# Performance work log

Measured on AMD Instinct MI355X. Metric: run time of the kernel, lower is better.

Reference implementation:

```python
import jax, jax.numpy as jnp
import numpy as np
import math

D_MODEL = 512
N_HEADS = 8
D_K = D_MODEL // N_HEADS
B, S, KC = 16, 1024, 32
NEG = -1e32


def setup_inputs() -> dict:
    key = jax.random.key(0)
    ks = jax.random.split(key, 14)
    s = 1.0 / math.sqrt(D_MODEL)
    return {
        "q": jax.random.normal(ks[0], (B, S, D_MODEL), jnp.float32),
        "k": jax.random.normal(ks[1], (B, S, D_MODEL), jnp.float32),
        "v": jax.random.normal(ks[2], (B, S, D_MODEL), jnp.float32),
        "q_seq": jax.random.randint(ks[3], (B, S), 0, 500, jnp.int32),
        "c_seq": jax.random.randint(ks[4], (B, S, KC), 0, 2, jnp.int32),
        "Wq": jax.random.normal(ks[5], (D_MODEL, D_MODEL), jnp.float32) * s,
        "bq": jnp.zeros((D_MODEL,), jnp.float32),
        "Wk": jax.random.normal(ks[6], (D_MODEL, D_MODEL), jnp.float32) * s,
        "bk": jnp.zeros((D_MODEL,), jnp.float32),
        "Wv": jax.random.normal(ks[7], (D_MODEL, D_MODEL), jnp.float32) * s,
        "bv": jnp.zeros((D_MODEL,), jnp.float32),
        "Wo": jax.random.normal(ks[8], (D_MODEL, D_MODEL), jnp.float32) * s,
        "bo": jnp.zeros((D_MODEL,), jnp.float32),
    }


def qc_mask(q_seq, c_seq):
    # maskq[b,i,j] = 1 if same question id
    maskq = (q_seq[:, :, None] == q_seq[:, None, :]).astype(jnp.int32)
    # maskc[b,i,j] = 1 if any shared concept; entries are {0,1} so AND-sum == dot
    overlap = jnp.einsum("bik,bjk->bij", c_seq, c_seq)  # int32
    maskc = (overlap > 0).astype(jnp.int32)
    # strict lower triangle: 1 - triu(ones, k=0)
    tri = jnp.tril(jnp.ones((S, S), jnp.int32), k=-1)[None]
    return (maskc + maskq + 1) * tri  # values in {0,1,2,3}


def reference(q, k, v, q_seq, c_seq, Wq, bq, Wk, bk, Wv, bv, Wo, bo):
    bs = q.shape[0]
    # NOTE: original code swaps the linears: k<-k_linear(k), q<-v_linear(q), v<-q_linear(v)
    kh = (k @ Wk.T + bk).reshape(bs, S, N_HEADS, D_K).transpose(0, 2, 1, 3)
    qh = (q @ Wv.T + bv).reshape(bs, S, N_HEADS, D_K).transpose(0, 2, 1, 3)
    vh = (v @ Wq.T + bq).reshape(bs, S, N_HEADS, D_K).transpose(0, 2, 1, 3)

    mask = qc_mask(q_seq, c_seq)  # [B,S,S] int
    scores = jnp.einsum("bhid,bhjd->bhij", qh, kh) / math.sqrt(D_K)
    m = mask[:, None]  # [B,1,S,S]
    scores = jnp.where(m == 0, NEG, scores)
    scores = jax.nn.softmax(scores, axis=-1)

    adjustments = jnp.array([0.0, 0.5, 1.0, 2.0], jnp.float32)
    adjusted = scores * adjustments[m]
    sums = jnp.sum(scores, axis=-1, keepdims=True)
    sums = jnp.where(sums == 0, jnp.ones_like(sums), sums)
    adjusted = adjusted / sums

    out = jnp.einsum("bhij,bhjd->bhid", adjusted, vh)
    concat = out.transpose(0, 2, 1, 3).reshape(bs, S, D_MODEL)
    return concat @ Wo.T + bo
```

## Files before the change

kernel.cpp:

```cpp
#include <hip/hip_runtime.h>
#include <stdint.h>

typedef unsigned short u16;
typedef unsigned int   u32;
typedef unsigned long long u64;
typedef __attribute__((ext_vector_type(8)))  short short8;
typedef __attribute__((ext_vector_type(4)))  float f32x4;
typedef __attribute__((ext_vector_type(16))) float f32x16;
typedef __attribute__((ext_vector_type(4)))  unsigned int u32x4;

__device__ __forceinline__ u16 f2bf(float f) {
  u32 u = __builtin_bit_cast(u32, f);
  u32 r = u + 0x7FFFu + ((u >> 16) & 1u);
  return (u16)(r >> 16);
}

__device__ __forceinline__ u32 cvtpk(float a, float b) {
  u32 r;
  asm("v_cvt_pk_bf16_f32 %0, %1, %2" : "=v"(r) : "v"(a), "v"(b));
  return r;
}

__device__ __forceinline__ void gload_lds16(const void* g, void* l) {
  __builtin_amdgcn_global_load_lds(
      (__attribute__((address_space(1))) void*)(uintptr_t)g,
      (__attribute__((address_space(3))) void*)(u32)(uintptr_t)l,
      16, 0, 0);
}

__global__ void cast4_kernel(const float* __restrict__ s0, const float* __restrict__ s1,
                             const float* __restrict__ s2, const float* __restrict__ s3,
                             u16* __restrict__ d0, u16* __restrict__ d1,
                             u16* __restrict__ d2, u16* __restrict__ d3, int n8) {
  const int sel = blockIdx.y;
  const float* src = sel == 0 ? s0 : sel == 1 ? s1 : sel == 2 ? s2 : s3;
  u16* dst = sel == 0 ? d0 : sel == 1 ? d1 : sel == 2 ? d2 : d3;
  int i = blockIdx.x * blockDim.x + threadIdx.x;
  if (i >= n8) return;
  const float4* s4 = (const float4*)src;
  float4 x = s4[2 * (size_t)i];
  float4 y = s4[2 * (size_t)i + 1];
  u32x4 r;
  r.x = cvtpk(x.x, x.y); r.y = cvtpk(x.z, x.w);
  r.z = cvtpk(y.x, y.y); r.w = cvtpk(y.z, y.w);
  *(u32x4*)(dst + 8 * (size_t)i) = r;
}

__global__ void pack_kernel(const int* __restrict__ q_seq, const int* __restrict__ c_seq,
                            int2* __restrict__ meta, int n) {
  int i = blockIdx.x * blockDim.x + threadIdx.x;
  if (i >= n) return;
  u32 bits = 0;
#pragma unroll
  for (int j = 0; j < 32; ++j)
    bits |= (c_seq[(size_t)i * 32 + j] != 0) ? (1u << j) : 0u;
  meta[i] = make_int2(q_seq[i], (int)bits);
}

__global__ __launch_bounds__(256) void mask_kernel(const int2* __restrict__ meta,
                                                   u64* __restrict__ maskw) {
  const int qc = blockIdx.x, kt = blockIdx.y, b = blockIdx.z;
  const int t = threadIdx.x;
  const int q = qc * 256 + t;
  __shared__ int2 colm[32];
  if (t < 32) colm[t] = meta[b * 1024 + kt * 32 + t];
  __syncthreads();
  const int2 qm = meta[b * 1024 + q];
  const int rs = qm.x; const u32 rb = (u32)qm.y;
  u64 w = 0;
#pragma unroll
  for (int j = 0; j < 32; ++j) {
    const int2 cm = colm[j];
    const int kj = kt * 32 + j;
    u32 m = 0;
    if (kj < q) m = 1u + (rs == cm.x ? 1u : 0u) + (((rb & (u32)cm.y) != 0u) ? 1u : 0u);
    w |= (u64)m << (2 * j);
  }
  maskw[((size_t)b * 32 + kt) * 1024 + q] = w;
}

__global__ __launch_bounds__(256) void gemm_qkv(const float* __restrict__ qf,
                                                const float* __restrict__ kf,
                                                const float* __restrict__ vf,
                                                const u16* __restrict__ Wvb,
                                                const u16* __restrict__ Wkb,
                                                const u16* __restrict__ Wqb,
                                                const float* __restrict__ bv,
                                                const float* __restrict__ bk,
                                                const float* __restrict__ bq,
                                                u16* __restrict__ qhb,
                                                u16* __restrict__ khb,
                                                u16* __restrict__ vTb,
                                                float kscale) {
  const int sel = blockIdx.y;
  const float* Af   = sel == 0 ? qf : sel == 1 ? kf : vf;
  const u16*   W    = sel == 0 ? Wvb : sel == 1 ? Wkb : Wqb;
  const float* bias = sel == 0 ? bv : sel == 1 ? bk : bq;
  const float scale = sel == 1 ? kscale : 1.0f;
  const int K = 512;

  __shared__ __align__(16) u16 As[128 * 64];
  __shared__ __align__(16) u16 Bs[128 * 64];
  const int t    = threadIdx.x;
  const int lane = t & 63;
  const int wid  = t >> 6;
  const int g    = lane >> 4, l15 = lane & 15;
  const int wm   = wid >> 1, wn = wid & 1;
  const int wrk  = (blockIdx.x & 7) * 64 + (blockIdx.x >> 3);
  const int mb   = wrk >> 2, nbi = wrk & 3;
  const int m0   = mb << 7, n0 = nbi << 7;
  const int srow = t >> 3;
  const int scol = (((t & 7) ^ (srow & 7)) << 3);
  const int rsw  = l15 & 7;

  f32x4 acc[4][4];
#pragma unroll
  for (int i = 0; i < 4; ++i)
#pragma unroll
    for (int j = 0; j < 4; ++j) acc[i][j] = f32x4{0.f, 0.f, 0.f, 0.f};

  float4 ax[4], ay[4];
#pragma unroll
  for (int i = 0; i < 4; ++i) {
    const float* src = Af + (size_t)(m0 + 32 * i + srow) * K + scol;
    ax[i] = *(const float4*)src;
    ay[i] = *(const float4*)(src + 4);
  }

  for (int k0 = 0; k0 < K; k0 += 64) {
    __builtin_amdgcn_sched_barrier(0);
    __builtin_amdgcn_s_barrier();
    __builtin_amdgcn_sched_barrier(0);
#pragma unroll
    for (int i = 0; i < 4; ++i)
      gload_lds16(W + (size_t)(n0 + i * 32 + srow) * K + k0 + scol,
                  Bs + i * 2048 + t * 8);
#pragma unroll
    for (int i = 0; i < 4; ++i) {
      u32x4 r;
      r.x = cvtpk(ax[i].x, ax[i].y); r.y = cvtpk(ax[i].z, ax[i].w);
      r.z = cvtpk(ay[i].x, ay[i].y); r.w = cvtpk(ay[i].z, ay[i].w);
      *(u32x4*)(As + (32 * i + srow) * 64 + ((t & 7) << 3)) = r;
    }
    __builtin_amdgcn_sched_barrier(0);
    const int kn = (k0 + 64) & (K - 1);
#pragma unroll
    for (int i = 0; i < 4; ++i) {
      const float* src = Af + (size_t)(m0 + 32 * i + srow) * K + kn + scol;
      ax[i] = *(const float4*)src;
      ay[i] = *(const float4*)(src + 4);
    }
    __builtin_amdgcn_sched_barrier(0);
    asm volatile("s_waitcnt vmcnt(8) lgkmcnt(0)" ::: "memory");
    __builtin_amdgcn_s_barrier();
    __builtin_amdgcn_sched_barrier(0);
#pragma unroll
    for (int kk = 0; kk < 2; ++kk) {
      short8 a[4], b[4];
#pragma unroll
      for (int mi = 0; mi < 4; ++mi)
        a[mi] = *(const short8*)(As + (wm * 64 + mi * 16 + l15) * 64
                                 + (((kk * 4 + g) ^ rsw) << 3));
#pragma unroll
      for (int ni = 0; ni < 4; ++ni)
        b[ni] = *(const short8*)(Bs + (wn * 64 + ni * 16 + l15) * 64
                                 + (((kk * 4 + g) ^ rsw) << 3));
#pragma unroll
      for (int mi = 0; mi < 4; ++mi)
#pragma unroll
        for (int ni = 0; ni < 4; ++ni)
          acc[mi][ni] = __builtin_amdgcn_mfma_f32_16x16x32_bf16(a[mi], b[ni], acc[mi][ni], 0, 0, 0);
    }
  }
  asm volatile("s_waitcnt vmcnt(0)" ::: "memory");

#pragma unroll
  for (int ni = 0; ni < 4; ++ni) {
    const int col = n0 + wn * 64 + ni * 16 + l15;
    const float bz = bias[col];
#pragma unroll
    for (int mi = 0; mi < 4; ++mi) {
#pragma unroll
      for (int r = 0; r < 4; ++r) {
        const int row = m0 + wm * 64 + mi * 16 + g * 4 + r;
        const u16 val = f2bf((acc[mi][ni][r] + bz) * scale);
        const size_t base = ((size_t)(row >> 10) * 8 + (col >> 6)) * 65536;
        const int s = row & 1023, d = col & 63;
        if (sel == 0) {
          qhb[base + (size_t)s * 64 + d] = val;
        } else if (sel == 1) {
          khb[base + (s >> 5) * 2048 + (d >> 3) * 256 + (s & 31) * 8 + (d & 7)] = val;
        } else {
          vTb[base + (s >> 3) * 512 + d * 8 + (s & 7)] = val;
        }
      }
    }
  }
}

__global__ __launch_bounds__(256) void gemm_out(const u16* __restrict__ A,
                                                const u16* __restrict__ W,
                                                const float* __restrict__ bias,
                                                float* __restrict__ outp) {
  const int K = 512, N = 512;
  __shared__ __align__(16) u16 As[128 * 64];
  __shared__ __align__(16) u16 Bs[128 * 64];
  const int t    = threadIdx.x;
  const int lane = t & 63;
  const int wid  = t >> 6;
  const int g    = lane >> 4, l15 = lane & 15;
  const int wm   = wid >> 1, wn = wid & 1;
  const int wrk  = (blockIdx.x & 7) * 64 + (blockIdx.x >> 3);
  const int mb   = wrk >> 2, nbi = wrk & 3;
  const int m0   = mb << 7, n0 = nbi << 7;
  const int srow = t >> 3;
  const int scol = (((t & 7) ^ (srow & 7)) << 3);
  const int rsw  = l15 & 7;

  f32x4 acc[4][4];
#pragma unroll
  for (int i = 0; i < 4; ++i)
#pragma unroll
    for (int j = 0; j < 4; ++j) acc[i][j] = f32x4{0.f, 0.f, 0.f, 0.f};

  for (int k0 = 0; k0 < K; k0 += 64) {
    __builtin_amdgcn_sched_barrier(0);
    __builtin_amdgcn_s_barrier();
    __builtin_amdgcn_sched_barrier(0);
#pragma unroll
    for (int i = 0; i < 4; ++i) {
      gload_lds16(A + (size_t)(m0 + i * 32 + srow) * K + k0 + scol, As + i * 2048 + t * 8);
      gload_lds16(W + (size_t)(n0 + i * 32 + srow) * K + k0 + scol, Bs + i * 2048 + t * 8);
    }
    __builtin_amdgcn_sched_barrier(0);
    asm volatile("s_waitcnt vmcnt(0)" ::: "memory");
    __builtin_amdgcn_s_barrier();
    __builtin_amdgcn_sched_barrier(0);
#pragma unroll
    for (int kk = 0; kk < 2; ++kk) {
      short8 a[4], b[4];
#pragma unroll
      for (int mi = 0; mi < 4; ++mi)
        a[mi] = *(const short8*)(As + (wm * 64 + mi * 16 + l15) * 64
                                 + (((kk * 4 + g) ^ rsw) << 3));
#pragma unroll
      for (int ni = 0; ni < 4; ++ni)
        b[ni] = *(const short8*)(Bs + (wn * 64 + ni * 16 + l15) * 64
                                 + (((kk * 4 + g) ^ rsw) << 3));
#pragma unroll
      for (int mi = 0; mi < 4; ++mi)
#pragma unroll
        for (int ni = 0; ni < 4; ++ni)
          acc[mi][ni] = __builtin_amdgcn_mfma_f32_16x16x32_bf16(a[mi], b[ni], acc[mi][ni], 0, 0, 0);
    }
  }

#pragma unroll
  for (int ni = 0; ni < 4; ++ni) {
    const int col = n0 + wn * 64 + ni * 16 + l15;
    const float bz = bias[col];
#pragma unroll
    for (int mi = 0; mi < 4; ++mi)
#pragma unroll
      for (int r = 0; r < 4; ++r) {
        const int row = m0 + wm * 64 + mi * 16 + g * 4 + r;
        outp[(size_t)row * N + col] = acc[mi][ni][r] + bz;
      }
  }
}

__global__ __launch_bounds__(256, 4) void attn_kernel(const u16* __restrict__ qh,
                                                      const u16* __restrict__ kh,
                                                      const u16* __restrict__ vT,
                                                      const u64* __restrict__ maskw,
                                                      u16* __restrict__ outc) {
  const int h  = blockIdx.x;
  const int qp = blockIdx.y;
  const int b  = blockIdx.z;
  const int lane = threadIdx.x & 63;
  const int wid  = threadIdx.x >> 6;
  const int pair = wid >> 1, p = wid & 1;
  const int l31 = lane & 31;
  const int hh  = lane >> 5;
  const int hh8 = hh << 3, fourh = hh << 2, eighth = hh << 3;
  const int jt = pair ? (31 - qp) : qp;
  const int q0 = jt << 5;
  const int qi = q0 + l31;
  const size_t bh = (size_t)b * 8 + h;
  const u16* Q  = qh + bh * 65536;
  const u16* Kp = kh + bh * 65536;
  const u16* Vt = vT + bh * 65536;
  const u64* mrow = maskw + (size_t)b * 32768 + qi;

  __shared__ float mO[2][32][64];
  __shared__ float mL[2][64];
  __shared__ __align__(16) float Sl[2][32];

  short8 qB[4];
#pragma unroll
  for (int i = 0; i < 4; ++i)
    qB[i] = *(const short8*)(Q + (size_t)qi * 64 + i * 16 + eighth);

  f32x16 O0, O1;
#pragma unroll
  for (int i = 0; i < 16; ++i) { O0[i] = 0.f; O1[i] = 0.f; }
  float lr[4] = {0.f, 0.f, 0.f, 0.f};

  const int nt = jt + 1;

  short8 kA[4];
#pragma unroll
  for (int i = 0; i < 4; ++i)
    kA[i] = *(const short8*)(Kp + p * 2048 + ((2 * i + hh) * 32 + l31) * 8);
  u64 wm = mrow[(size_t)p << 10];

  for (int t = p; t < nt; t += 2) {
    const int k0 = t << 5;

    f32x16 S;
#pragma unroll
    for (int i = 0; i < 16; ++i) S[i] = 0.f;
#pragma unroll
    for (int i = 0; i < 4; ++i)
      S = __builtin_amdgcn_mfma_f32_32x32x16_bf16(kA[i], qB[i], S, 0, 0, 0);

    u64 wmn = 0;
    if (t + 2 < nt) {
#pragma unroll
      for (int i = 0; i < 4; ++i)
        kA[i] = *(const short8*)(Kp + (t + 2) * 2048 + ((2 * i + hh) * 32 + l31) * 8);
      wmn = mrow[(size_t)(t + 2) << 10];
    }

    short8 vB[2][2];
#pragma unroll
    for (int t4 = 0; t4 < 2; ++t4)
#pragma unroll
      for (int j = 0; j < 2; ++j)
        vB[t4][j] = *(const short8*)(Vt + (size_t)(t * 4 + t4 * 2 + hh) * 512 + (32 * j + l31) * 8);

    const u32 wsh0 = ((u32)wm) >> hh8;
    const u32 wsh1 = ((u32)(wm >> 32)) >> hh8;
    u32 pk[8];
#pragma unroll
    for (int s = 0; s < 4; ++s) {
      const u32 wsel = (s < 2) ? wsh0 : wsh1;
      float pv[4];
#pragma unroll
      for (int r = 0; r < 4; ++r) {
        const int m = 4 * s + r;
        const u32 m2 = (wsel >> (2 * r + 16 * (s & 1))) & 3u;
        float e;
        asm("v_exp_f32 %0, %1" : "=v"(e) : "v"(S[m]));
        const float pp = (m2 != 0u) ? e : 0.f;
        lr[r] += pp;
        asm("v_ldexp_f32 %0, %1, %2" : "=v"(pv[r]) : "v"(pp), "v"(m2));
      }
      pk[2 * s]     = cvtpk(pv[0], pv[1]);
      pk[2 * s + 1] = cvtpk(pv[2], pv[3]);
    }
    wm = wmn;

#pragma unroll
    for (int t4 = 0; t4 < 2; ++t4) {
      u32 a0 = pk[4 * t4 + 0], b0 = pk[4 * t4 + 2];
      u32 a1 = pk[4 * t4 + 1], b1 = pk[4 * t4 + 3];
      asm("v_permlane32_swap_b32 %0, %1" : "+v"(a0), "+v"(b0));
      asm("v_permlane32_swap_b32 %0, %1" : "+v"(a1), "+v"(b1));
      u32x4 w; w.x = a0; w.y = a1; w.z = b0; w.w = b1;
      const short8 pa = __builtin_bit_cast(short8, w);
      O0 = __builtin_amdgcn_mfma_f32_32x32x16_bf16(pa, vB[t4][0], O0, 0, 0, 0);
      O1 = __builtin_amdgcn_mfma_f32_32x32x16_bf16(pa, vB[t4][1], O1, 0, 0, 0);
    }
  }

  float lrun = (lr[0] + lr[1]) + (lr[2] + lr[3]);

  if (p == 1) {
#pragma unroll
    for (int r = 0; r < 16; ++r) {
      mO[pair][r][lane]      = O0[r];
      mO[pair][16 + r][lane] = O1[r];
    }
    mL[pair][lane] = lrun;
  }
  __syncthreads();
  if (p == 0) {
#pragma unroll
    for (int r = 0; r < 16; ++r) {
      O0[r] += mO[pair][r][lane];
      O1[r] += mO[pair][16 + r][lane];
    }
    lrun += mL[pair][lane];

    const float ssum = lrun + __shfl_xor(lrun, 32);
    if (lane < 32) Sl[pair][l31] = (ssum > 0.f) ? 0.25f / ssum : 0.f;
    __builtin_amdgcn_sched_barrier(0);
    asm volatile("s_waitcnt lgkmcnt(0)" ::: "memory");
    __builtin_amdgcn_sched_barrier(0);
#pragma unroll
    for (int t2 = 0; t2 < 4; ++t2) {
      const float4 inv4 = *(const float4*)&Sl[pair][8 * t2 + fourh];
#pragma unroll
      for (int r = 0; r < 4; ++r) {
        const int m = 4 * t2 + r;
        const float iv = (r == 0) ? inv4.x : (r == 1) ? inv4.y : (r == 2) ? inv4.z : inv4.w;
        const int qrow = q0 + 8 * t2 + fourh + r;
        u16* op = outc + ((size_t)b * 1024 + qrow) * 512 + h * 64;
        op[l31]      = f2bf(O0[m] * iv);
        op[32 + l31] = f2bf(O1[m] * iv);
      }
    }
  }
}

extern "C" void kernel_launch(void* const* d_in, const int* in_sizes, int n_in,
                              void* d_out, int out_size, void* d_ws, size_t ws_size,
                              hipStream_t stream) {
  (void)in_sizes; (void)n_in; (void)out_size; (void)ws_size;
  const float* q    = (const float*)d_in[0];
  const float* k    = (const float*)d_in[1];
  const float* v    = (const float*)d_in[2];
  const int*  q_seq = (const int*)d_in[3];
  const int*  c_seq = (const int*)d_in[4];
  const float* Wq   = (const float*)d_in[5];
  const float* bq   = (const float*)d_in[6];
  const float* Wk   = (const float*)d_in[7];
  const float* bk   = (const float*)d_in[8];
  const float* Wv   = (const float*)d_in[9];
  const float* bv   = (const float*)d_in[10];
  const float* Wo   = (const float*)d_in[11];
  const float* bo   = (const float*)d_in[12];
  float* out = (float*)d_out;

  char* ws = (char*)d_ws;
  const size_t SZH = 16ull * 8 * 1024 * 64 * 2;
  u16* qhb   = (u16*)(ws + 0 * SZH);
  u16* khb   = (u16*)(ws + 1 * SZH);
  u16* vTb   = (u16*)(ws + 2 * SZH);
  u16* attnc = (u16*)(ws + 3 * SZH);
  u16* Wvb = (u16*)(ws + 4 * SZH + 0 * 524288);
  u16* Wkb = (u16*)(ws + 4 * SZH + 1 * 524288);
  u16* Wqb = (u16*)(ws + 4 * SZH + 2 * 524288);
  u16* Wob = (u16*)(ws + 4 * SZH + 3 * 524288);
  int2* meta  = (int2*)(ws + 4 * SZH + 4 * 524288);
  u64* maskw  = (u64*)(ws + 4 * SZH + 4 * 524288 + 131072);

  const int n8w = 512 * 512 / 8;
  cast4_kernel<<<dim3(n8w / 256, 4), 256, 0, stream>>>(Wv, Wk, Wq, Wo,
                                                       Wvb, Wkb, Wqb, Wob, n8w);
  pack_kernel<<<64, 256, 0, stream>>>(q_seq, c_seq, meta, 16384);
  mask_kernel<<<dim3(4, 32, 16), 256, 0, stream>>>(meta, maskw);

  const float KSCALE = 0.18033688011112042f;
  gemm_qkv<<<dim3(512, 3), 256, 0, stream>>>(q, k, v, Wvb, Wkb, Wqb,
                                             bv, bk, bq, qhb, khb, vTb, KSCALE);
  attn_kernel<<<dim3(8, 16, 16), 256, 0, stream>>>(qhb, khb, vTb, maskw, attnc);
  gemm_out<<<512, 256, 0, stream>>>(attnc, Wob, bo, out);
}
```

Before: 142.6 us.

## Double-buffer LDS tiles in QKV and output projection GEMMs

Both projection GEMMs now keep two LDS buffers for the A and B tiles. The next k-tile's global-to-LDS loads are issued before the MFMAs on the current tile, so each iteration needs one barrier instead of two. This is meant to hide global load latency behind matrix math. In exchange, LDS use per block doubles to 64 KB, which may lower occupancy.

After: 145.1 us. Within noise of the previous version (+1.8%).

```diff
diff --git a/kernel.cpp b/kernel.cpp
--- a/kernel.cpp
+++ b/kernel.cpp
@@ -27,6 +27,8 @@
       (__attribute__((address_space(3))) void*)(u32)(uintptr_t)l,
       16, 0, 0);
 }
+
+#define SB() __builtin_amdgcn_sched_barrier(0)
 
 __global__ void cast4_kernel(const float* __restrict__ s0, const float* __restrict__ s1,
                              const float* __restrict__ s2, const float* __restrict__ s3,
@@ -99,8 +101,8 @@
   const float scale = sel == 1 ? kscale : 1.0f;
   const int K = 512;
 
-  __shared__ __align__(16) u16 As[128 * 64];
-  __shared__ __align__(16) u16 Bs[128 * 64];
+  __shared__ __align__(16) u16 As[2][128 * 64];
+  __shared__ __align__(16) u16 Bs[2][128 * 64];
   const int t    = threadIdx.x;
   const int lane = t & 63;
   const int wid  = t >> 6;
@@ -111,6 +113,7 @@
   const int m0   = mb << 7, n0 = nbi << 7;
   const int srow = t >> 3;
   const int scol = (((t & 7) ^ (srow & 7)) << 3);
+  const int dcol = ((t & 7) << 3);
   const int rsw  = l15 & 7;
 
   f32x4 acc[4][4];
@@ -126,51 +129,97 @@
     ax[i] = *(const float4*)src;
     ay[i] = *(const float4*)(src + 4);
   }
-
-  for (int k0 = 0; k0 < K; k0 += 64) {
-    __builtin_amdgcn_sched_barrier(0);
-    __builtin_amdgcn_s_barrier();
-    __builtin_amdgcn_sched_barrier(0);
+  SB();
+#pragma unroll
+  for (int i = 0; i < 4; ++i)
+    gload_lds16(W + (size_t)(n0 + i * 32 + srow) * K + scol, &Bs[0][i * 2048 + t * 8]);
+  SB();
+  asm volatile("s_waitcnt vmcnt(4)" ::: "memory");
+#pragma unroll
+  for (int i = 0; i < 4; ++i) {
+    u32x4 r;
+    r.x = cvtpk(ax[i].x, ax[i].y); r.y = cvtpk(ax[i].z, ax[i].w);
+    r.z = cvtpk(ay[i].x, ay[i].y); r.w = cvtpk(ay[i].z, ay[i].w);
+    *(u32x4*)(&As[0][(32 * i + srow) * 64 + dcol]) = r;
+  }
+  SB();
+#pragma unroll
+  for (int i = 0; i < 4; ++i) {
+    const float* src = Af + (size_t)(m0 + 32 * i + srow) * K + 64 + scol;
+    ax[i] = *(const float4*)src;
+    ay[i] = *(const float4*)(src + 4);
+  }
+  SB();
+  asm volatile("s_waitcnt vmcnt(8) lgkmcnt(0)" ::: "memory");
+  __builtin_amdgcn_s_barrier();
+  SB();
+
+  for (int tt = 0; tt < 7; ++tt) {
+    const int c = tt & 1;
+    const u16* Asc = As[c];
+    const u16* Bsc = Bs[c];
+    u16* Asn = As[c ^ 1];
+    u16* Bsn = Bs[c ^ 1];
 #pragma unroll
     for (int i = 0; i < 4; ++i)
-      gload_lds16(W + (size_t)(n0 + i * 32 + srow) * K + k0 + scol,
-                  Bs + i * 2048 + t * 8);
+      gload_lds16(W + (size_t)(n0 + i * 32 + srow) * K + (tt + 1) * 64 + scol,
+                  Bsn + i * 2048 + t * 8);
+    SB();
 #pragma unroll
     for (int i = 0; i < 4; ++i) {
       u32x4 r;
       r.x = cvtpk(ax[i].x, ax[i].y); r.y = cvtpk(ax[i].z, ax[i].w);
       r.z = cvtpk(ay[i].x, ay[i].y); r.w = cvtpk(ay[i].z, ay[i].w);
-      *(u32x4*)(As + (32 * i + srow) * 64 + ((t & 7) << 3)) = r;
-    }
-    __builtin_amdgcn_sched_barrier(0);
-    const int kn = (k0 + 64) & (K - 1);
+      *(u32x4*)(Asn + (32 * i + srow) * 64 + dcol) = r;
+    }
+    SB();
+    const int kn = ((tt + 2) & 7) * 64;
 #pragma unroll
     for (int i = 0; i < 4; ++i) {
       const float* src = Af + (size_t)(m0 + 32 * i + srow) * K + kn + scol;
       ax[i] = *(const float4*)src;
       ay[i] = *(const float4*)(src + 4);
     }
-    __builtin_amdgcn_sched_barrier(0);
+    SB();
+#pragma unroll
+    for (int kk = 0; kk < 2; ++kk) {
+      short8 a[4], b[4];
+#pragma unroll
+      for (int mi = 0; mi < 4; ++mi)
+        a[mi] = *(const short8*)(Asc + (wm * 64 + mi * 16 + l15) * 64
+                                 + (((kk * 4 + g) ^ rsw) << 3));
+#pragma unroll
+      for (int ni = 0; ni < 4; ++ni)
+        b[ni] = *(const short8*)(Bsc + (wn * 64 + ni * 16 + l15) * 64
+                                 + (((kk * 4 + g) ^ rsw) << 3));
+#pragma unroll
+      for (int mi = 0; mi < 4; ++mi)
+#pragma unroll
+        for (int ni = 0; ni < 4; ++ni)
+          acc[mi][ni] = __builtin_amdgcn_mfma_f32_16x16x32_bf16(a[mi], b[ni], acc[mi][ni], 0, 0, 0);
+    }
+    SB();
     asm volatile("s_waitcnt vmcnt(8) lgkmcnt(0)" ::: "memory");
     __builtin_amdgcn_s_barrier();
-    __builtin_amdgcn_sched_barrier(0);
-#pragma unroll
-    for (int kk = 0; kk < 2; ++kk) {
-      short8 a[4], b[4];
-#pragma unroll
-      for (int mi = 0; mi < 4; ++mi)
-        a[mi] = *(const short8*)(As + (wm * 64 + mi * 16 + l15) * 64
-                                 + (((kk * 4 + g) ^ rsw) << 3));
+    SB();
+  }
+
+#pragma unroll
+  for (int kk = 0; kk < 2; ++kk) {
+    short8 a[4], b[4];
+#pragma unroll
+    for (int mi = 0; mi < 4; ++mi)
+      a[mi] = *(const short8*)(&As[1][(wm * 64 + mi * 16 + l15) * 64
+                               + (((kk * 4 + g) ^ rsw) << 3)]);
+#pragma unroll
+    for (int ni = 0; ni < 4; ++ni)
+      b[ni] = *(const short8*)(&Bs[1][(wn * 64 + ni * 16 + l15) * 64
+                               + (((kk * 4 + g) ^ rsw) << 3)]);
+#pragma unroll
+    for (int mi = 0; mi < 4; ++mi)
 #pragma unroll
       for (int ni = 0; ni < 4; ++ni)
-        b[ni] = *(const short8*)(Bs + (wn * 64 + ni * 16 + l15) * 64
-                                 + (((kk * 4 + g) ^ rsw) << 3));
-#pragma unroll
-      for (int mi = 0; mi < 4; ++mi)
-#pragma unroll
-        for (int ni = 0; ni < 4; ++ni)
-          acc[mi][ni] = __builtin_amdgcn_mfma_f32_16x16x32_bf16(a[mi], b[ni], acc[mi][ni], 0, 0, 0);
-    }
+        acc[mi][ni] = __builtin_amdgcn_mfma_f32_16x16x32_bf16(a[mi], b[ni], acc[mi][ni], 0, 0, 0);
   }
   asm volatile("s_waitcnt vmcnt(0)" ::: "memory");
 
@@ -203,8 +252,8 @@
                                                 const float* __restrict__ bias,
                                                 float* __restrict__ outp) {
   const int K = 512, N = 512;
-  __shared__ __align__(16) u16 As[128 * 64];
-  __shared__ __align__(16) u16 Bs[128 * 64];
+  __shared__ __align__(16) u16 As[2][128 * 64];
+  __shared__ __align__(16) u16 Bs[2][128 * 64];
   const int t    = threadIdx.x;
   const int lane = t & 63;
   const int wid  = t >> 6;
@@ -223,29 +272,40 @@
 #pragma unroll
     for (int j = 0; j < 4; ++j) acc[i][j] = f32x4{0.f, 0.f, 0.f, 0.f};
 
-  for (int k0 = 0; k0 < K; k0 += 64) {
-    __builtin_amdgcn_sched_barrier(0);
-    __builtin_amdgcn_s_barrier();
-    __builtin_amdgcn_sched_barrier(0);
+#pragma unroll
+  for (int i = 0; i < 4; ++i) {
+    gload_lds16(A + (size_t)(m0 + i * 32 + srow) * K + scol, &As[0][i * 2048 + t * 8]);
+    gload_lds16(W + (size_t)(n0 + i * 32 + srow) * K + scol, &Bs[0][i * 2048 + t * 8]);
+  }
+  SB();
+  asm volatile("s_waitcnt vmcnt(0)" ::: "memory");
+  __builtin_amdgcn_s_barrier();
+  SB();
+
+  for (int tt = 0; tt < 7; ++tt) {
+    const int c = tt & 1;
+    const u16* Asc = As[c];
+    const u16* Bsc = Bs[c];
+    u16* Asn = As[c ^ 1];
+    u16* Bsn = Bs[c ^ 1];
 #pragma unroll
     for (int i = 0; i < 4; ++i) {
-      gload_lds16(A + (size_t)(m0 + i * 32 + srow) * K + k0 + scol, As + i * 2048 + t * 8);
-      gload_lds16(W + (size_t)(n0 + i * 32 + srow) * K + k0 + scol, Bs + i * 2048 + t * 8);
-    }
-    __builtin_amdgcn_sched_barrier(0);
-    asm volatile("s_waitcnt vmcnt(0)" ::: "memory");
-    __builtin_amdgcn_s_barrier();
-    __builtin_amdgcn_sched_barrier(0);
+      gload_lds16(A + (size_t)(m0 + i * 32 + srow) * K + (tt + 1) * 64 + scol,
+                  Asn + i * 2048 + t * 8);
+      gload_lds16(W + (size_t)(n0 + i * 32 + srow) * K + (tt + 1) * 64 + scol,
+                  Bsn + i * 2048 + t * 8);
+    }
+    SB();
 #pragma unroll
     for (int kk = 0; kk < 2; ++kk) {
       short8 a[4], b[4];
 #pragma unroll
       for (int mi = 0; mi < 4; ++mi)
-        a[mi] = *(const short8*)(As + (wm * 64 + mi * 16 + l15) * 64
+        a[mi] = *(const short8*)(Asc + (wm * 64 + mi * 16 + l15) * 64
                                  + (((kk * 4 + g) ^ rsw) << 3));
 #pragma unroll
       for (int ni = 0; ni < 4; ++ni)
-        b[ni] = *(const short8*)(Bs + (wn * 64 + ni * 16 + l15) * 64
+        b[ni] = *(const short8*)(Bsc + (wn * 64 + ni * 16 + l15) * 64
                                  + (((kk * 4 + g) ^ rsw) << 3));
 #pragma unroll
       for (int mi = 0; mi < 4; ++mi)
@@ -253,6 +313,28 @@
         for (int ni = 0; ni < 4; ++ni)
           acc[mi][ni] = __builtin_amdgcn_mfma_f32_16x16x32_bf16(a[mi], b[ni], acc[mi][ni], 0, 0, 0);
     }
+    SB();
+    asm volatile("s_waitcnt vmcnt(0) lgkmcnt(0)" ::: "memory");
+    __builtin_amdgcn_s_barrier();
+    SB();
+  }
+
+#pragma unroll
+  for (int kk = 0; kk < 2; ++kk) {
+    short8 a[4], b[4];
+#pragma unroll
+    for (int mi = 0; mi < 4; ++mi)
+      a[mi] = *(const short8*)(&As[1][(wm * 64 + mi * 16 + l15) * 64
+                               + (((kk * 4 + g) ^ rsw) << 3)]);
+#pragma unroll
+    for (int ni = 0; ni < 4; ++ni)
+      b[ni] = *(const short8*)(&Bs[1][(wn * 64 + ni * 16 + l15) * 64
+                               + (((kk * 4 + g) ^ rsw) << 3)]);
+#pragma unroll
+    for (int mi = 0; mi < 4; ++mi)
+#pragma unroll
+      for (int ni = 0; ni < 4; ++ni)
+        acc[mi][ni] = __builtin_amdgcn_mfma_f32_16x16x32_bf16(a[mi], b[ni], acc[mi][ni], 0, 0, 0);
   }
 
 #pragma unroll
```

## Process two key tiles per attention loop iteration with double-buffered K loads

Applied to the files above, without the earlier changes.

The attention inner loop now handles two key tiles (t and t+2) per iteration, with separate K-fragment and mask buffers, and prefetches the next pair before the softmax and PV work. V fragments are now loaded inside the PV step instead of up front. The aim is more independent MFMA and exp work in flight to hide load and dependency latency. To fit the extra registers, launch bounds drop from 4 to 2 blocks per CU, which risks lower occupancy. Adding the SB() macro and hoisting the store column into dcol are cosmetic.

Result: no change. 140.1 us (-1.7%).

```diff
diff --git a/kernel.cpp b/kernel.cpp
--- a/kernel.cpp
+++ b/kernel.cpp
@@ -27,6 +27,8 @@
       (__attribute__((address_space(3))) void*)(u32)(uintptr_t)l,
       16, 0, 0);
 }
+
+#define SB() __builtin_amdgcn_sched_barrier(0)
 
 __global__ void cast4_kernel(const float* __restrict__ s0, const float* __restrict__ s1,
                              const float* __restrict__ s2, const float* __restrict__ s3,
@@ -111,6 +113,7 @@
   const int m0   = mb << 7, n0 = nbi << 7;
   const int srow = t >> 3;
   const int scol = (((t & 7) ^ (srow & 7)) << 3);
+  const int dcol = ((t & 7) << 3);
   const int rsw  = l15 & 7;
 
   f32x4 acc[4][4];
@@ -128,9 +131,9 @@
   }
 
   for (int k0 = 0; k0 < K; k0 += 64) {
-    __builtin_amdgcn_sched_barrier(0);
+    SB();
     __builtin_amdgcn_s_barrier();
-    __builtin_amdgcn_sched_barrier(0);
+    SB();
 #pragma unroll
     for (int i = 0; i < 4; ++i)
       gload_lds16(W + (size_t)(n0 + i * 32 + srow) * K + k0 + scol,
@@ -140,9 +143,9 @@
       u32x4 r;
       r.x = cvtpk(ax[i].x, ax[i].y); r.y = cvtpk(ax[i].z, ax[i].w);
       r.z = cvtpk(ay[i].x, ay[i].y); r.w = cvtpk(ay[i].z, ay[i].w);
-      *(u32x4*)(As + (32 * i + srow) * 64 + ((t & 7) << 3)) = r;
-    }
-    __builtin_amdgcn_sched_barrier(0);
+      *(u32x4*)(As + (32 * i + srow) * 64 + dcol) = r;
+    }
+    SB();
     const int kn = (k0 + 64) & (K - 1);
 #pragma unroll
     for (int i = 0; i < 4; ++i) {
@@ -150,10 +153,10 @@
       ax[i] = *(const float4*)src;
       ay[i] = *(const float4*)(src + 4);
     }
-    __builtin_amdgcn_sched_barrier(0);
+    SB();
     asm volatile("s_waitcnt vmcnt(8) lgkmcnt(0)" ::: "memory");
     __builtin_amdgcn_s_barrier();
-    __builtin_amdgcn_sched_barrier(0);
+    SB();
 #pragma unroll
     for (int kk = 0; kk < 2; ++kk) {
       short8 a[4], b[4];
@@ -224,18 +227,18 @@
     for (int j = 0; j < 4; ++j) acc[i][j] = f32x4{0.f, 0.f, 0.f, 0.f};
 
   for (int k0 = 0; k0 < K; k0 += 64) {
-    __builtin_amdgcn_sched_barrier(0);
+    SB();
     __builtin_amdgcn_s_barrier();
-    __builtin_amdgcn_sched_barrier(0);
+    SB();
 #pragma unroll
     for (int i = 0; i < 4; ++i) {
       gload_lds16(A + (size_t)(m0 + i * 32 + srow) * K + k0 + scol, As + i * 2048 + t * 8);
       gload_lds16(W + (size_t)(n0 + i * 32 + srow) * K + k0 + scol, Bs + i * 2048 + t * 8);
     }
-    __builtin_amdgcn_sched_barrier(0);
+    SB();
     asm volatile("s_waitcnt vmcnt(0)" ::: "memory");
     __builtin_amdgcn_s_barrier();
-    __builtin_amdgcn_sched_barrier(0);
+    SB();
 #pragma unroll
     for (int kk = 0; kk < 2; ++kk) {
       short8 a[4], b[4];
@@ -269,7 +272,7 @@
   }
 }
 
-__global__ __launch_bounds__(256, 4) void attn_kernel(const u16* __restrict__ qh,
+__global__ __launch_bounds__(256, 2) void attn_kernel(const u16* __restrict__ qh,
                                                       const u16* __restrict__ kh,
                                                       const u16* __restrict__ vT,
                                                       const u64* __restrict__ maskw,
@@ -308,71 +311,97 @@
 
   const int nt = jt + 1;
 
-  short8 kA[4];
-#pragma unroll
-  for (int i = 0; i < 4; ++i)
-    kA[i] = *(const short8*)(Kp + p * 2048 + ((2 * i + hh) * 32 + l31) * 8);
-  u64 wm = mrow[(size_t)p << 10];
-
-  for (int t = p; t < nt; t += 2) {
-    const int k0 = t << 5;
-
-    f32x16 S;
-#pragma unroll
-    for (int i = 0; i < 16; ++i) S[i] = 0.f;
+#define LOADK(dst, tt)                                                        \
+  { _Pragma("unroll")                                                         \
+    for (int i = 0; i < 4; ++i)                                               \
+      dst[i] = *(const short8*)(Kp + (tt) * 2048 + ((2 * i + hh) * 32 + l31) * 8); }
+
+#define SOFTMAX(S, wm, pkk)                                                   \
+  { const u32 wsh0 = ((u32)(wm)) >> hh8;                                      \
+    const u32 wsh1 = ((u32)((wm) >> 32)) >> hh8;                              \
+    _Pragma("unroll")                                                         \
+    for (int s = 0; s < 4; ++s) {                                             \
+      const u32 wsel = (s < 2) ? wsh0 : wsh1;                                 \
+      float pv[4];                                                            \
+      _Pragma("unroll")                                                       \
+      for (int r = 0; r < 4; ++r) {                                           \
+        const int m = 4 * s + r;                                              \
+        const u32 m2 = (wsel >> (2 * r + 16 * (s & 1))) & 3u;                 \
+        float e;                                                              \
+        asm("v_exp_f32 %0, %1" : "=v"(e) : "v"((S)[m]));                      \
+        const float pp = (m2 != 0u) ? e : 0.f;                                \
+        lr[r] += pp;                                                          \
+        asm("v_ldexp_f32 %0, %1, %2" : "=v"(pv[r]) : "v"(pp), "v"(m2));       \
+      }                                                                       \
+      pkk[2 * s]     = cvtpk(pv[0], pv[1]);                                   \
+      pkk[2 * s + 1] = cvtpk(pv[2], pv[3]);                                   \
+    } }
+
+#define PVSTEP(pkk, tt)                                                       \
+  { _Pragma("unroll")                                                         \
+    for (int t4 = 0; t4 < 2; ++t4) {                                          \
+      u32 a0 = pkk[4 * t4 + 0], b0 = pkk[4 * t4 + 2];                         \
+      u32 a1 = pkk[4 * t4 + 1], b1 = pkk[4 * t4 + 3];                         \
+      asm("v_permlane32_swap_b32 %0, %1" : "+v"(a0), "+v"(b0));               \
+      asm("v_permlane32_swap_b32 %0, %1" : "+v"(a1), "+v"(b1));               \
+      u32x4 w; w.x = a0; w.y = a1; w.z = b0; w.w = b1;                        \
+      const short8 pa = __builtin_bit_cast(short8, w);                        \
+      const short8 v0 = *(const short8*)(Vt + (size_t)((tt) * 4 + t4 * 2 + hh) * 512 + l31 * 8); \
+      const short8 v1 = *(const short8*)(Vt + (size_t)((tt) * 4 + t4 * 2 + hh) * 512 + (32 + l31) * 8); \
+      O0 = __builtin_amdgcn_mfma_f32_32x32x16_bf16(pa, v0, O0, 0, 0, 0);      \
+      O1 = __builtin_amdgcn_mfma_f32_32x32x16_bf16(pa, v1, O1, 0, 0, 0);      \
+    } }
+
+  short8 kAa[4], kAb[4];
+  LOADK(kAa, p);
+  LOADK(kAb, (p + 2));
+  u64 wma = mrow[(size_t)p << 10];
+  u64 wmb = mrow[(size_t)(p + 2) << 10];
+
+  int t = p;
+  while (t < nt) {
+    const bool two = (t + 2) < nt;
+
+    f32x16 Sa;
+#pragma unroll
+    for (int i = 0; i < 16; ++i) Sa[i] = 0.f;
 #pragma unroll
     for (int i = 0; i < 4; ++i)
-      S = __builtin_amdgcn_mfma_f32_32x32x16_bf16(kA[i], qB[i], S, 0, 0, 0);
-
-    u64 wmn = 0;
-    if (t + 2 < nt) {
+      Sa = __builtin_amdgcn_mfma_f32_32x32x16_bf16(kAa[i], qB[i], Sa, 0, 0, 0);
+    f32x16 Sb;
+#pragma unroll
+    for (int i = 0; i < 16; ++i) Sb[i] = 0.f;
+    if (two) {
 #pragma unroll
       for (int i = 0; i < 4; ++i)
-        kA[i] = *(const short8*)(Kp + (t + 2) * 2048 + ((2 * i + hh) * 32 + l31) * 8);
-      wmn = mrow[(size_t)(t + 2) << 10];
-    }
-
-    short8 vB[2][2];
-#pragma unroll
-    for (int t4 = 0; t4 < 2; ++t4)
-#pragma unroll
-      for (int j = 0; j < 2; ++j)
-        vB[t4][j] = *(const short8*)(Vt + (size_t)(t * 4 + t4 * 2 + hh) * 512 + (32 * j + l31) * 8);
-
-    const u32 wsh0 = ((u32)wm) >> hh8;
-    const u32 wsh1 = ((u32)(wm >> 32)) >> hh8;
-    u32 pk[8];
-#pragma unroll
-    for (int s = 0; s < 4; ++s) {
-      const u32 wsel = (s < 2) ? wsh0 : wsh1;
-      float pv[4];
-#pragma unroll
-      for (int r = 0; r < 4; ++r) {
-        const int m = 4 * s + r;
-        const u32 m2 = (wsel >> (2 * r + 16 * (s & 1))) & 3u;
-        float e;
-        asm("v_exp_f32 %0, %1" : "=v"(e) : "v"(S[m]));
-        const float pp = (m2 != 0u) ? e : 0.f;
-        lr[r] += pp;
-        asm("v_ldexp_f32 %0, %1, %2" : "=v"(pv[r]) : "v"(pp), "v"(m2));
+        Sb = __builtin_amdgcn_mfma_f32_32x32x16_bf16(kAb[i], qB[i], Sb, 0, 0, 0);
+    }
+
+    const int tn = t + (two ? 4 : 2);
+    u64 wman = 0, wmbn = 0;
+    if (tn < nt) {
+      LOADK(kAa, tn);
+      wman = mrow[(size_t)tn << 10];
+      if (tn + 2 < nt) {
+        LOADK(kAb, (tn + 2));
+        wmbn = mrow[(size_t)(tn + 2) << 10];
       }
-      pk[2 * s]     = cvtpk(pv[0], pv[1]);
-      pk[2 * s + 1] = cvtpk(pv[2], pv[3]);
-    }
-    wm = wmn;
-
-#pragma unroll
-    for (int t4 = 0; t4 < 2; ++t4) {
-      u32 a0 = pk[4 * t4 + 0], b0 = pk[4 * t4 + 2];
-      u32 a1 = pk[4 * t4 + 1], b1 = pk[4 * t4 + 3];
-      asm("v_permlane32_swap_b32 %0, %1" : "+v"(a0), "+v"(b0));
-      asm("v_permlane32_swap_b32 %0, %1" : "+v"(a1), "+v"(b1));
-      u32x4 w; w.x = a0; w.y = a1; w.z = b0; w.w = b1;
-      const short8 pa = __builtin_bit_cast(short8, w);
-      O0 = __builtin_amdgcn_mfma_f32_32x32x16_bf16(pa, vB[t4][0], O0, 0, 0, 0);
-      O1 = __builtin_amdgcn_mfma_f32_32x32x16_bf16(pa, vB[t4][1], O1, 0, 0, 0);
-    }
-  }
+    }
+
+    u32 pka[8], pkb[8];
+    SOFTMAX(Sa, wma, pka);
+    if (two) SOFTMAX(Sb, wmb, pkb);
+
+    PVSTEP(pka, t);
+    if (two) PVSTEP(pkb, (t + 2));
+
+    wma = wman; wmb = wmbn;
+    t = tn;
+  }
+
+#undef LOADK
+#undef SOFTMAX
+#undef PVSTEP
 
   float lrun = (lr[0] + lr[1]) + (lr[2] + lr[3]);
 
```
